# Kernel optimization log

Measured on AMD Instinct MI355X. Metric: run time of the kernel, lower is better.

Reference implementation:

```python
import jax, jax.numpy as jnp
import numpy as np

E = 500_000
N = 30_000
R = 6
H = 256
OE = 256
OUT = 1
L = 3          # num_layers
A = 2          # num_aux + 1 branches


def setup_inputs() -> dict:
    key = jax.random.key(0)
    ks = jax.random.split(key, 9)
    x = jax.random.normal(ks[0], (E, H), dtype=jnp.float32)
    rbf = jax.random.normal(ks[1], (E, R), dtype=jnp.float32)
    i = jax.random.randint(ks[2], (E,), 0, N, dtype=jnp.int64)
    # parameters (stored in [in, out] convention)
    s = 1.0 / np.sqrt(H)
    W_rbf = jax.random.normal(ks[3], (R, H), dtype=jnp.float32) / np.sqrt(R)
    W_up = jax.random.normal(ks[4], (A, H, OE), dtype=jnp.float32) * s
    W_hidden = jax.random.normal(ks[5], (A, L, OE, OE), dtype=jnp.float32) / np.sqrt(OE)
    b_hidden = jnp.zeros((A, L, OE), dtype=jnp.float32)
    W_out = jax.random.normal(ks[6], (A, OE, OUT), dtype=jnp.float32) / np.sqrt(OE)
    return {"x": x, "rbf": rbf, "i": i, "num_nodes": N,
            "W_rbf": W_rbf, "W_up": W_up, "W_hidden": W_hidden,
            "b_hidden": b_hidden, "W_out": W_out}


def reference(x, rbf, i, num_nodes, W_rbf, W_up, W_hidden, b_hidden, W_out):
    # elementwise multiply of per-edge features by radial basis projection,
    # then segment-sum over edge target index -> per-node features [N, H]
    msg = (rbf @ W_rbf) * x                     # [E, H]
    h = jax.ops.segment_sum(msg, i, num_segments=num_nodes)  # [N, H]
    outs = []
    for a in range(A):
        y = h @ W_up[a]                          # [N, OE]
        for l in range(L):
            y = jax.nn.silu(y @ W_hidden[a, l] + b_hidden[a, l])
        outs.append(y @ W_out[a])               # [N, OUT]
    return tuple(outs)
```

## Files before the change

### kernel.cpp

```cpp
#include <hip/hip_runtime.h>

#define E_EDGES 500000
#define N_NODES 30000
#define H_DIM   256

typedef float  floatx4 __attribute__((ext_vector_type(4)));
typedef float  floatx2 __attribute__((ext_vector_type(2)));
typedef short  shortx4 __attribute__((ext_vector_type(4)));
typedef short  shortx8 __attribute__((ext_vector_type(8)));
typedef __bf16 bf16x8  __attribute__((ext_vector_type(8)));

__device__ inline short f2bf(float f) {
    unsigned u = __builtin_bit_cast(unsigned, f);
    u += 0x7fffu + ((u >> 16) & 1u);
    return (short)(u >> 16);
}
__device__ inline float bf2f(short s) {
    unsigned u = ((unsigned)(unsigned short)s) << 16;
    return __builtin_bit_cast(float, u);
}

__global__ __launch_bounds__(256) void prep_hist(
    const float* __restrict__ wup, const float* __restrict__ whid,
    short* __restrict__ wfrag,
    const int* __restrict__ idx, int* __restrict__ counts)
{
    const int b = blockIdx.x;
    if (b < 256) {
        int g   = b * 256 + threadIdx.x;
        int mat = g >> 13;
        int grp = g & 8191;
        int a = mat >> 2, lay = mat & 3;
        const float* src = (lay == 0) ? (wup + a * 65536)
                                      : (whid + (a * 3 + lay - 1) * 65536);
        int ks  = grp >> 10;
        int rem = grp & 1023;
        int ntg = rem >> 6;
        int lane = rem & 63;
        int q = lane >> 4, c = lane & 15;
        int col = ntg * 16 + c;
        int k0  = ks * 32 + q * 8;
        shortx8 v;
#pragma unroll
        for (int j = 0; j < 8; j++) v[j] = f2bf(src[(k0 + j) * 256 + col]);
        ((shortx8*)wfrag)[g] = v;
    } else {
        int g = (b - 256) * 256 + threadIdx.x;
        if (g < E_EDGES / 4) {
            int4 v = ((const int4*)idx)[g];
            atomicAdd(&counts[v.x], 1);
            atomicAdd(&counts[v.y], 1);
            atomicAdd(&counts[v.z], 1);
            atomicAdd(&counts[v.w], 1);
        }
    }
}

__global__ __launch_bounds__(1024) void scan_kernel(
    const int* __restrict__ counts, int* __restrict__ offsets,
    int* __restrict__ cursor)
{
    const int t = threadIdx.x;
    const int lane = t & 63, wave = t >> 6;
    const int base = t * 30;
    int local[30];
    int s = 0;
#pragma unroll
    for (int j = 0; j < 30; j++) {
        int c = (base + j < N_NODES) ? counts[base + j] : 0;
        local[j] = s;
        s += c;
    }
    int incl = s;
#pragma unroll
    for (int d = 1; d < 64; d <<= 1) {
        int v = __shfl_up(incl, d);
        if (lane >= d) incl += v;
    }
    __shared__ int part[16];
    if (lane == 63) part[wave] = incl;
    __syncthreads();
    if (t == 0) {
        int run = 0;
#pragma unroll
        for (int k = 0; k < 16; k++) { int v = part[k]; part[k] = run; run += v; }
    }
    __syncthreads();
    int excl = part[wave] + incl - s;
#pragma unroll
    for (int j = 0; j < 30; j++) {
        int n = base + j;
        if (n < N_NODES) { offsets[n] = excl + local[j]; cursor[n] = excl + local[j]; }
    }
    if (t == 1023) offsets[N_NODES] = E_EDGES;
}

__global__ __launch_bounds__(256) void scatter_ids(
    const int* __restrict__ idx, int* __restrict__ cursor,
    int* __restrict__ edge_list)
{
    int g = blockIdx.x * 256 + threadIdx.x;
    if (g >= E_EDGES / 4) return;
    int4 v = ((const int4*)idx)[g];
    int e0 = g * 4;
    int p0 = atomicAdd(&cursor[v.x], 1); edge_list[p0] = e0 + 0;
    int p1 = atomicAdd(&cursor[v.y], 1); edge_list[p1] = e0 + 1;
    int p2 = atomicAdd(&cursor[v.z], 1); edge_list[p2] = e0 + 2;
    int p3 = atomicAdd(&cursor[v.w], 1); edge_list[p3] = e0 + 3;
}

__global__ __launch_bounds__(256) void gather_nodes(
    const float* __restrict__ x, const float* __restrict__ rbf,
    const int* __restrict__ edge_list, const int* __restrict__ offsets,
    const float* __restrict__ wrbf, short* __restrict__ h16)
{
    int node = blockIdx.x * 4 + (threadIdx.x >> 6);
    if (node >= N_NODES) return;
    int lane = threadIdx.x & 63;

    const floatx4* wr4 = (const floatx4*)wrbf;
    floatx4 wr[6];
#pragma unroll
    for (int k = 0; k < 6; k++) wr[k] = wr4[k * 64 + lane];

    int beg = offsets[node], end = offsets[node + 1];
    floatx4 acc = {0.f, 0.f, 0.f, 0.f};
    for (int j0 = beg; j0 < end; j0 += 64) {
        int myid = (j0 + lane < end)
                 ? __builtin_nontemporal_load(&edge_list[j0 + lane]) : 0;
        int cnt  = end - j0; if (cnt > 64) cnt = 64;
#pragma unroll 2
        for (int g = 0; g < cnt; g++) {
            int e = __shfl(myid, g);
            const float* rp = rbf + e * 6;
            floatx2 r01 = __builtin_nontemporal_load((const floatx2*)(rp + 0));
            floatx2 r23 = __builtin_nontemporal_load((const floatx2*)(rp + 2));
            floatx2 r45 = __builtin_nontemporal_load((const floatx2*)(rp + 4));
            floatx4 xv = __builtin_nontemporal_load(
                &((const floatx4*)x)[(size_t)e * 64 + lane]);
            floatx4 p = r01[0] * wr[0] + r01[1] * wr[1] + r23[0] * wr[2]
                      + r23[1] * wr[3] + r45[0] * wr[4] + r45[1] * wr[5];
            acc += p * xv;
        }
    }
    shortx4 s4 = { f2bf(acc.x), f2bf(acc.y), f2bf(acc.z), f2bf(acc.w) };
    ((shortx4*)h16)[(size_t)node * 64 + lane] = s4;
}

__global__ __launch_bounds__(256, 2) void mlp_kernel(
    const short* __restrict__ h16, const short* __restrict__ wfrag,
    const float* __restrict__ bias, const float* __restrict__ wout,
    float* __restrict__ out)
{
    __shared__ __align__(16) short ylds[64 * 264];
    const int t = threadIdx.x;
    const int wave = t >> 6, lane = t & 63, q = lane >> 4, c15 = lane & 15;
    const int a  = blockIdx.x & 1;
    const int n0 = (blockIdx.x >> 1) * 64;

#pragma unroll
    for (int j = 0; j < 8; j++) {
        int grp = t + j * 256;
        int r = grp >> 5, c8 = grp & 31;
        shortx8 v = {0, 0, 0, 0, 0, 0, 0, 0};
        if (n0 + r < N_NODES)
            v = *(const shortx8*)&h16[(size_t)(n0 + r) * 256 + c8 * 8];
        *(shortx8*)&ylds[r * 264 + c8 * 8] = v;
    }
    __syncthreads();

    for (int lay = 0; lay < 4; lay++) {
        const bf16x8* wf = (const bf16x8*)(wfrag + (size_t)(a * 4 + lay) * 65536);
        floatx4 acc[4][4];
#pragma unroll
        for (int mt = 0; mt < 4; mt++)
#pragma unroll
            for (int nt = 0; nt < 4; nt++)
                acc[mt][nt] = (floatx4){0.f, 0.f, 0.f, 0.f};

#pragma unroll
        for (int ks = 0; ks < 8; ks++) {
            bf16x8 bfr[4];
#pragma unroll
            for (int nt = 0; nt < 4; nt++)
                bfr[nt] = wf[(ks * 16 + wave * 4 + nt) * 64 + lane];
#pragma unroll
            for (int mt = 0; mt < 4; mt++) {
                bf16x8 afr = *(const bf16x8*)&ylds[(mt * 16 + c15) * 264 + ks * 32 + q * 8];
#pragma unroll
                for (int nt = 0; nt < 4; nt++)
                    acc[mt][nt] = __builtin_amdgcn_mfma_f32_16x16x32_bf16(
                        afr, bfr[nt], acc[mt][nt], 0, 0, 0);
            }
        }
        __syncthreads();

        float bv[4];
#pragma unroll
        for (int nt = 0; nt < 4; nt++)
            bv[nt] = (lay >= 1)
                   ? bias[(a * 3 + lay - 1) * 256 + wave * 64 + nt * 16 + c15]
                   : 0.0f;
#pragma unroll
        for (int mt = 0; mt < 4; mt++)
#pragma unroll
            for (int nt = 0; nt < 4; nt++)
#pragma unroll
                for (int rg = 0; rg < 4; rg++) {
                    float v = acc[mt][nt][rg] + bv[nt];
                    if (lay >= 1) v = v / (1.0f + __expf(-v));
                    ylds[(mt * 16 + q * 4 + rg) * 264 + wave * 64 + nt * 16 + c15] = f2bf(v);
                }
        __syncthreads();
    }

    {
        int r  = wave * 16 + (lane >> 2);
        int cq = lane & 3;
        const float* wo = wout + a * 256 + cq * 64;
        const short* yp = &ylds[r * 264 + cq * 64];
        float s = 0.0f;
#pragma unroll
        for (int bb = 0; bb < 8; bb++) {
            shortx8 v = *(const shortx8*)&yp[bb * 8];
#pragma unroll
            for (int j = 0; j < 8; j++) s += bf2f(v[j]) * wo[bb * 8 + j];
        }
        s += __shfl_xor(s, 1);
        s += __shfl_xor(s, 2);
        if (cq == 0 && n0 + r < N_NODES) out[a * N_NODES + n0 + r] = s;
    }
}

extern "C" void kernel_launch(void* const* d_in, const int* in_sizes, int n_in,
                              void* d_out, int out_size, void* d_ws, size_t ws_size,
                              hipStream_t stream)
{
    (void)in_sizes; (void)n_in; (void)out_size; (void)ws_size;
    const float* x    = (const float*)d_in[0];
    const float* rbf  = (const float*)d_in[1];
    const int*   idx  = (const int*)d_in[2];
    const float* wrbf = (const float*)d_in[4];
    const float* wup  = (const float*)d_in[5];
    const float* whid = (const float*)d_in[6];
    const float* bias = (const float*)d_in[7];
    const float* wout = (const float*)d_in[8];
    float* out = (float*)d_out;

    char* ws = (char*)d_ws;
    short* h16       = (short*)ws;  ws += (size_t)N_NODES * H_DIM * sizeof(short);
    short* wfrag     = (short*)ws;  ws += (size_t)8 * 65536 * sizeof(short);
    int*   counts    = (int*)ws;    ws += (size_t)N_NODES * sizeof(int);
    int*   offsets   = (int*)ws;    ws += (size_t)(N_NODES + 1) * sizeof(int);
    int*   cursor    = (int*)ws;    ws += (size_t)N_NODES * sizeof(int);
    int*   edge_list = (int*)ws;

    hipMemsetAsync(counts, 0, (size_t)N_NODES * sizeof(int), stream);
    prep_hist<<<256 + (E_EDGES / 4 + 255) / 256, 256, 0, stream>>>(
        wup, whid, wfrag, idx, counts);
    scan_kernel<<<1, 1024, 0, stream>>>(counts, offsets, cursor);
    scatter_ids<<<(E_EDGES / 4 + 255) / 256, 256, 0, stream>>>(idx, cursor, edge_list);
    gather_nodes<<<(N_NODES + 3) / 4, 256, 0, stream>>>(x, rbf, edge_list, offsets, wrbf, h16);
    mlp_kernel<<<938, 256, 0, stream>>>(h16, wfrag, bias, wout, out);
}
```

Baseline: 828.5 us.

## Split scatter/gather by node range to overlap scatter with gather

The edge scatter is split into two node ranges. The second half of the scatter runs in the same launch as the gather for the first half, so the irregular atomic scatter overlaps with bandwidth-heavy gathering. The scan now reads counts with vectorized int4 loads. The MLP kernel processes both branches per block, reusing the loaded node tile coordinates but halving block count. The change adds extra idx reads and launches, and each block now carries a longer serial MLP chain.

```diff
diff --git a/kernel.cpp b/kernel.cpp
--- a/kernel.cpp
+++ b/kernel.cpp
@@ -3,6 +3,8 @@
 #define E_EDGES 500000
 #define N_NODES 30000
 #define H_DIM   256
+#define SPLIT_N 14976
+#define SCAT_BLOCKS 489
 
 typedef float  floatx4 __attribute__((ext_vector_type(4)));
 typedef float  floatx2 __attribute__((ext_vector_type(2)));
@@ -62,14 +64,26 @@
 {
     const int t = threadIdx.x;
     const int lane = t & 63, wave = t >> 6;
-    const int base = t * 30;
-    int local[30];
+    const int base = t * 32;
+    int local[32];
     int s = 0;
-#pragma unroll
-    for (int j = 0; j < 30; j++) {
-        int c = (base + j < N_NODES) ? counts[base + j] : 0;
-        local[j] = s;
-        s += c;
+    if (base < N_NODES) {
+#pragma unroll
+        for (int q4 = 0; q4 < 8; q4++) {
+            int4 v = ((const int4*)counts)[t * 8 + q4];
+            int i0 = base + q4 * 4;
+            int c0 = (i0 + 0 < N_NODES) ? v.x : 0;
+            int c1 = (i0 + 1 < N_NODES) ? v.y : 0;
+            int c2 = (i0 + 2 < N_NODES) ? v.z : 0;
+            int c3 = (i0 + 3 < N_NODES) ? v.w : 0;
+            local[i0 - base + 0] = s; s += c0;
+            local[i0 - base + 1] = s; s += c1;
+            local[i0 - base + 2] = s; s += c2;
+            local[i0 - base + 3] = s; s += c3;
+        }
+    } else {
+#pragma unroll
+        for (int j = 0; j < 32; j++) local[j] = 0;
     }
     int incl = s;
 #pragma unroll
@@ -88,35 +102,43 @@
     __syncthreads();
     int excl = part[wave] + incl - s;
 #pragma unroll
-    for (int j = 0; j < 30; j++) {
+    for (int j = 0; j < 32; j++) {
         int n = base + j;
-        if (n < N_NODES) { offsets[n] = excl + local[j]; cursor[n] = excl + local[j]; }
-    }
-    if (t == 1023) offsets[N_NODES] = E_EDGES;
-}
-
-__global__ __launch_bounds__(256) void scatter_ids(
-    const int* __restrict__ idx, int* __restrict__ cursor,
-    int* __restrict__ edge_list)
-{
-    int g = blockIdx.x * 256 + threadIdx.x;
+        if (n < N_NODES) { int o = excl + local[j]; offsets[n] = o; cursor[n] = o; }
+    }
+    if (t == 0) offsets[N_NODES] = E_EDGES;
+}
+
+__device__ inline void scatter_body(
+    int g, const int* __restrict__ idx, int* __restrict__ cursor,
+    int* __restrict__ edge_list, int lo, int hi)
+{
     if (g >= E_EDGES / 4) return;
     int4 v = ((const int4*)idx)[g];
     int e0 = g * 4;
-    int p0 = atomicAdd(&cursor[v.x], 1); edge_list[p0] = e0 + 0;
-    int p1 = atomicAdd(&cursor[v.y], 1); edge_list[p1] = e0 + 1;
-    int p2 = atomicAdd(&cursor[v.z], 1); edge_list[p2] = e0 + 2;
-    int p3 = atomicAdd(&cursor[v.w], 1); edge_list[p3] = e0 + 3;
-}
-
-__global__ __launch_bounds__(256) void gather_nodes(
+    if (v.x >= lo && v.x < hi) { int p = atomicAdd(&cursor[v.x], 1); edge_list[p] = e0 + 0; }
+    if (v.y >= lo && v.y < hi) { int p = atomicAdd(&cursor[v.y], 1); edge_list[p] = e0 + 1; }
+    if (v.z >= lo && v.z < hi) { int p = atomicAdd(&cursor[v.z], 1); edge_list[p] = e0 + 2; }
+    if (v.w >= lo && v.w < hi) { int p = atomicAdd(&cursor[v.w], 1); edge_list[p] = e0 + 3; }
+}
+
+__global__ __launch_bounds__(256) void scatter_lo(
+    const int* __restrict__ idx, int* __restrict__ cursor,
+    int* __restrict__ edge_list)
+{
+    scatter_body(blockIdx.x * 256 + threadIdx.x, idx, cursor, edge_list, 0, SPLIT_N);
+}
+
+__device__ inline void gather_body(
+    int blk, int tid,
     const float* __restrict__ x, const float* __restrict__ rbf,
     const int* __restrict__ edge_list, const int* __restrict__ offsets,
-    const float* __restrict__ wrbf, short* __restrict__ h16)
-{
-    int node = blockIdx.x * 4 + (threadIdx.x >> 6);
-    if (node >= N_NODES) return;
-    int lane = threadIdx.x & 63;
+    const float* __restrict__ wrbf, short* __restrict__ h16,
+    int node_base, int node_cnt)
+{
+    int node = node_base + blk * 4 + (tid >> 6);
+    if (node >= node_base + node_cnt || node >= N_NODES) return;
+    int lane = tid & 63;
 
     const floatx4* wr4 = (const floatx4*)wrbf;
     floatx4 wr[6];
@@ -147,6 +169,31 @@
     ((shortx4*)h16)[(size_t)node * 64 + lane] = s4;
 }
 
+__global__ __launch_bounds__(256) void scatterB_gatherA(
+    const int* __restrict__ idx, int* __restrict__ cursor,
+    int* __restrict__ edge_list,
+    const float* __restrict__ x, const float* __restrict__ rbf,
+    const int* __restrict__ offsets, const float* __restrict__ wrbf,
+    short* __restrict__ h16)
+{
+    if (blockIdx.x < SCAT_BLOCKS) {
+        scatter_body(blockIdx.x * 256 + threadIdx.x, idx, cursor, edge_list,
+                     SPLIT_N, N_NODES);
+    } else {
+        gather_body(blockIdx.x - SCAT_BLOCKS, threadIdx.x,
+                    x, rbf, edge_list, offsets, wrbf, h16, 0, SPLIT_N);
+    }
+}
+
+__global__ __launch_bounds__(256) void gather_hi(
+    const float* __restrict__ x, const float* __restrict__ rbf,
+    const int* __restrict__ edge_list, const int* __restrict__ offsets,
+    const float* __restrict__ wrbf, short* __restrict__ h16)
+{
+    gather_body(blockIdx.x, threadIdx.x, x, rbf, edge_list, offsets, wrbf, h16,
+                SPLIT_N, N_NODES - SPLIT_N);
+}
+
 __global__ __launch_bounds__(256, 2) void mlp_kernel(
     const short* __restrict__ h16, const short* __restrict__ wfrag,
     const float* __restrict__ bias, const float* __restrict__ wout,
@@ -155,80 +202,82 @@
     __shared__ __align__(16) short ylds[64 * 264];
     const int t = threadIdx.x;
     const int wave = t >> 6, lane = t & 63, q = lane >> 4, c15 = lane & 15;
-    const int a  = blockIdx.x & 1;
-    const int n0 = (blockIdx.x >> 1) * 64;
-
-#pragma unroll
-    for (int j = 0; j < 8; j++) {
-        int grp = t + j * 256;
-        int r = grp >> 5, c8 = grp & 31;
-        shortx8 v = {0, 0, 0, 0, 0, 0, 0, 0};
-        if (n0 + r < N_NODES)
-            v = *(const shortx8*)&h16[(size_t)(n0 + r) * 256 + c8 * 8];
-        *(shortx8*)&ylds[r * 264 + c8 * 8] = v;
-    }
-    __syncthreads();
-
-    for (int lay = 0; lay < 4; lay++) {
-        const bf16x8* wf = (const bf16x8*)(wfrag + (size_t)(a * 4 + lay) * 65536);
-        floatx4 acc[4][4];
-#pragma unroll
-        for (int mt = 0; mt < 4; mt++)
+    const int n0 = blockIdx.x * 64;
+
+    for (int a = 0; a < 2; a++) {
+#pragma unroll
+        for (int j = 0; j < 8; j++) {
+            int grp = t + j * 256;
+            int r = grp >> 5, c8 = grp & 31;
+            shortx8 v = {0, 0, 0, 0, 0, 0, 0, 0};
+            if (n0 + r < N_NODES)
+                v = *(const shortx8*)&h16[(size_t)(n0 + r) * 256 + c8 * 8];
+            *(shortx8*)&ylds[r * 264 + c8 * 8] = v;
+        }
+        __syncthreads();
+
+        for (int lay = 0; lay < 4; lay++) {
+            const bf16x8* wf = (const bf16x8*)(wfrag + (size_t)(a * 4 + lay) * 65536);
+            floatx4 acc[4][4];
+#pragma unroll
+            for (int mt = 0; mt < 4; mt++)
+#pragma unroll
+                for (int nt = 0; nt < 4; nt++)
+                    acc[mt][nt] = (floatx4){0.f, 0.f, 0.f, 0.f};
+
+#pragma unroll
+            for (int ks = 0; ks < 8; ks++) {
+                bf16x8 bfr[4];
+#pragma unroll
+                for (int nt = 0; nt < 4; nt++)
+                    bfr[nt] = wf[(ks * 16 + wave * 4 + nt) * 64 + lane];
+#pragma unroll
+                for (int mt = 0; mt < 4; mt++) {
+                    bf16x8 afr = *(const bf16x8*)&ylds[(mt * 16 + c15) * 264 + ks * 32 + q * 8];
+#pragma unroll
+                    for (int nt = 0; nt < 4; nt++)
+                        acc[mt][nt] = __builtin_amdgcn_mfma_f32_16x16x32_bf16(
+                            afr, bfr[nt], acc[mt][nt], 0, 0, 0);
+                }
+            }
+            __syncthreads();
+
+            float bv[4];
 #pragma unroll
             for (int nt = 0; nt < 4; nt++)
-                acc[mt][nt] = (floatx4){0.f, 0.f, 0.f, 0.f};
-
-#pragma unroll
-        for (int ks = 0; ks < 8; ks++) {
-            bf16x8 bfr[4];
-#pragma unroll
-            for (int nt = 0; nt < 4; nt++)
-                bfr[nt] = wf[(ks * 16 + wave * 4 + nt) * 64 + lane];
-#pragma unroll
-            for (int mt = 0; mt < 4; mt++) {
-                bf16x8 afr = *(const bf16x8*)&ylds[(mt * 16 + c15) * 264 + ks * 32 + q * 8];
+                bv[nt] = (lay >= 1)
+                       ? bias[(a * 3 + lay - 1) * 256 + wave * 64 + nt * 16 + c15]
+                       : 0.0f;
+#pragma unroll
+            for (int mt = 0; mt < 4; mt++)
 #pragma unroll
                 for (int nt = 0; nt < 4; nt++)
-                    acc[mt][nt] = __builtin_amdgcn_mfma_f32_16x16x32_bf16(
-                        afr, bfr[nt], acc[mt][nt], 0, 0, 0);
+#pragma unroll
+                    for (int rg = 0; rg < 4; rg++) {
+                        float v = acc[mt][nt][rg] + bv[nt];
+                        if (lay >= 1) v = v / (1.0f + __expf(-v));
+                        ylds[(mt * 16 + q * 4 + rg) * 264 + wave * 64 + nt * 16 + c15] = f2bf(v);
+                    }
+            __syncthreads();
+        }
+
+        {
+            int r  = wave * 16 + (lane >> 2);
+            int cq = lane & 3;
+            const float* wo = wout + a * 256 + cq * 64;
+            const short* yp = &ylds[r * 264 + cq * 64];
+            float s = 0.0f;
+#pragma unroll
+            for (int bb = 0; bb < 8; bb++) {
+                shortx8 v = *(const shortx8*)&yp[bb * 8];
+#pragma unroll
+                for (int j = 0; j < 8; j++) s += bf2f(v[j]) * wo[bb * 8 + j];
             }
+            s += __shfl_xor(s, 1);
+            s += __shfl_xor(s, 2);
+            if (cq == 0 && n0 + r < N_NODES) out[a * N_NODES + n0 + r] = s;
         }
         __syncthreads();
-
-        float bv[4];
-#pragma unroll
-        for (int nt = 0; nt < 4; nt++)
-            bv[nt] = (lay >= 1)
-                   ? bias[(a * 3 + lay - 1) * 256 + wave * 64 + nt * 16 + c15]
-                   : 0.0f;
-#pragma unroll
-        for (int mt = 0; mt < 4; mt++)
-#pragma unroll
-            for (int nt = 0; nt < 4; nt++)
-#pragma unroll
-                for (int rg = 0; rg < 4; rg++) {
-                    float v = acc[mt][nt][rg] + bv[nt];
-                    if (lay >= 1) v = v / (1.0f + __expf(-v));
-                    ylds[(mt * 16 + q * 4 + rg) * 264 + wave * 64 + nt * 16 + c15] = f2bf(v);
-                }
-        __syncthreads();
-    }
-
-    {
-        int r  = wave * 16 + (lane >> 2);
-        int cq = lane & 3;
-        const float* wo = wout + a * 256 + cq * 64;
-        const short* yp = &ylds[r * 264 + cq * 64];
-        float s = 0.0f;
-#pragma unroll
-        for (int bb = 0; bb < 8; bb++) {
-            shortx8 v = *(const shortx8*)&yp[bb * 8];
-#pragma unroll
-            for (int j = 0; j < 8; j++) s += bf2f(v[j]) * wo[bb * 8 + j];
-        }
-        s += __shfl_xor(s, 1);
-        s += __shfl_xor(s, 2);
-        if (cq == 0 && n0 + r < N_NODES) out[a * N_NODES + n0 + r] = s;
     }
 }
 
@@ -256,10 +305,12 @@
     int*   edge_list = (int*)ws;
 
     hipMemsetAsync(counts, 0, (size_t)N_NODES * sizeof(int), stream);
-    prep_hist<<<256 + (E_EDGES / 4 + 255) / 256, 256, 0, stream>>>(
-        wup, whid, wfrag, idx, counts);
+    prep_hist<<<256 + SCAT_BLOCKS, 256, 0, stream>>>(wup, whid, wfrag, idx, counts);
     scan_kernel<<<1, 1024, 0, stream>>>(counts, offsets, cursor);
-    scatter_ids<<<(E_EDGES / 4 + 255) / 256, 256, 0, stream>>>(idx, cursor, edge_list);
-    gather_nodes<<<(N_NODES + 3) / 4, 256, 0, stream>>>(x, rbf, edge_list, offsets, wrbf, h16);
-    mlp_kernel<<<938, 256, 0, stream>>>(h16, wfrag, bias, wout, out);
-}
+    scatter_lo<<<SCAT_BLOCKS, 256, 0, stream>>>(idx, cursor, edge_list);
+    scatterB_gatherA<<<SCAT_BLOCKS + SPLIT_N / 4, 256, 0, stream>>>(
+        idx, cursor, edge_list, x, rbf, offsets, wrbf, h16);
+    gather_hi<<<(N_NODES - SPLIT_N) / 4, 256, 0, stream>>>(
+        x, rbf, edge_list, offsets, wrbf, h16);
+    mlp_kernel<<<(N_NODES + 63) / 64, 256, 0, stream>>>(h16, wfrag, bias, wout, out);
+}
```

Measured after the change: 846.8 us. +2.2%, slower.
